# Kernel optimization log

Hardware: AMD Instinct MI355X
Metric: run time of the kernel (lower is better)

## Reference

```python
import jax, jax.numpy as jnp
import numpy as np

B, L, D, H, DH, M = 2, 2048, 512, 8, 2048, 128  # batch, seq, d_model, heads, d_hidden, max_rel_pos
HD = D // H
EPS = 1e-5


def _ln(x, w, b):
    mu = jnp.mean(x, axis=-1, keepdims=True)
    var = jnp.mean((x - mu) ** 2, axis=-1, keepdims=True)
    return (x - mu) * jax.lax.rsqrt(var + EPS) * w + b


def setup_inputs() -> dict:
    key = jax.random.key(0)
    ks = jax.random.split(key, 8)
    s = 0.02  # init std for weights
    return {
        "x": jax.random.normal(ks[0], (B, L, D), jnp.float32),
        "ln1_w": jnp.ones((D,), jnp.float32),
        "ln1_b": jnp.zeros((D,), jnp.float32),
        "qkv_w": jax.random.normal(ks[1], (D, 3 * D), jnp.float32) * s,
        "qkv_b": jnp.zeros((3 * D,), jnp.float32),
        "out_w": jax.random.normal(ks[2], (D, D), jnp.float32) * s,
        "out_b": jnp.zeros((D,), jnp.float32),
        "rel_bias": jax.random.normal(ks[3], (H, 2 * M - 1), jnp.float32) * s,
        "gamma1": 1e-4 * jnp.ones((D,), jnp.float32),
        "ln2_w": jnp.ones((D,), jnp.float32),
        "ln2_b": jnp.zeros((D,), jnp.float32),
        "ffn_in_w": jax.random.normal(ks[4], (D, 2 * DH), jnp.float32) * s,
        "ffn_in_b": jnp.zeros((2 * DH,), jnp.float32),
        "ffn_out_w": jax.random.normal(ks[5], (DH, D), jnp.float32) * s,
        "ffn_out_b": jnp.zeros((D,), jnp.float32),
        "gamma2": 1e-4 * jnp.ones((D,), jnp.float32),
    }


def _forward(x, ln1_w, ln1_b, qkv_w, qkv_b, out_w, out_b, rel_bias, gamma1,
             ln2_w, ln2_b, ffn_in_w, ffn_in_b, ffn_out_w, ffn_out_b, gamma2):
    b, l, d = x.shape
    # --- PreNorm attention with T5-style relative position bias ---
    h = _ln(x, ln1_w, ln1_b)
    qkv = h @ qkv_w + qkv_b                           # [B, L, 3D]
    q, k, v = jnp.split(qkv, 3, axis=-1)
    q = q.reshape(b, l, H, HD)
    k = k.reshape(b, l, H, HD)
    v = v.reshape(b, l, H, HD)
    scale = 1.0 / jnp.sqrt(jnp.asarray(HD, x.dtype))
    scores = jnp.einsum("bqhd,bkhd->bhqk", q, k) * scale   # [B, H, L, L]
    # relative position bias: clip(i - j) indexed into learned table
    ctx = jnp.arange(l)[:, None] - jnp.arange(l)[None, :]
    ctx = jnp.clip(ctx, -(M - 1), M - 1) + (M - 1)          # [L, L] in [0, 2M-2]
    rel = rel_bias[:, ctx]                                  # [H, L, L]
    scores = scores + rel[None]
    attn = jax.nn.softmax(scores, axis=-1)
    o = jnp.einsum("bhqk,bkhd->bqhd", attn, v).reshape(b, l, d)
    o = o @ out_w + out_b
    x = x + o * gamma1                                      # LayerScale residual
    # --- PreNorm GEGLU FFN ---
    h2 = _ln(x, ln2_w, ln2_b)
    ab = h2 @ ffn_in_w + ffn_in_b                           # [B, L, 2*DH]
    a, bgate = jnp.split(ab, 2, axis=-1)
    f = jax.nn.gelu(bgate, approximate=False) * a
    f = f @ ffn_out_w + ffn_out_b
    x = x + f * gamma2
    return x, attn


def reference(x, ln1_w, ln1_b, qkv_w, qkv_b, out_w, out_b, rel_bias, gamma1,
              ln2_w, ln2_b, ffn_in_w, ffn_in_b, ffn_out_w, ffn_out_b, gamma2):
    return _forward(x, ln1_w, ln1_b, qkv_w, qkv_b, out_w, out_b, rel_bias, gamma1,
                    ln2_w, ln2_b, ffn_in_w, ffn_in_b, ffn_out_w, ffn_out_b, gamma2)
```

## Files before the change

### kernel.cpp

```cpp
#include <hip/hip_runtime.h>
#include <math.h>

typedef __attribute__((ext_vector_type(4))) float f32x4;
typedef __attribute__((ext_vector_type(8))) short bf16x8;
typedef __attribute__((ext_vector_type(4))) short s16x4;

__device__ __forceinline__ unsigned short f2bf(float f) {
  union { float f; unsigned u; } v; v.f = f;
  return (unsigned short)((v.u + 0x7fffu + ((v.u >> 16) & 1u)) >> 16);
}

__global__ void ln_kernel(const float* __restrict__ in, const float* __restrict__ w,
                          const float* __restrict__ b, float* __restrict__ out) {
  __shared__ float sh[4];
  const int t = threadIdx.x;
  const float* p = in + (size_t)blockIdx.x * 512;
  float a0 = p[t], a1 = p[t + 256];
  float s = a0 + a1;
#pragma unroll
  for (int o = 32; o; o >>= 1) s += __shfl_down(s, o);
  if ((t & 63) == 0) sh[t >> 6] = s;
  __syncthreads();
  s = sh[0] + sh[1] + sh[2] + sh[3];
  float mu = s * (1.0f / 512.0f);
  float d0 = a0 - mu, d1 = a1 - mu;
  float q = d0 * d0 + d1 * d1;
  __syncthreads();
#pragma unroll
  for (int o = 32; o; o >>= 1) q += __shfl_down(q, o);
  if ((t & 63) == 0) sh[t >> 6] = q;
  __syncthreads();
  q = sh[0] + sh[1] + sh[2] + sh[3];
  float rstd = rsqrtf(q * (1.0f / 512.0f) + 1e-5f);
  float* po = out + (size_t)blockIdx.x * 512;
  po[t]       = d0 * rstd * w[t] + b[t];
  po[t + 256] = d1 * rstd * w[t + 256] + b[t + 256];
}

__global__ void transpose_w(const float* __restrict__ in, unsigned short* __restrict__ out,
                            int ldi, int ldo, long ibs, long obs) {
  __shared__ float tile[32][33];
  const float* ip = in + (long)blockIdx.z * ibs;
  unsigned short* op = out + (long)blockIdx.z * obs;
  const int tx = threadIdx.x & 31;
  const int ty = threadIdx.x >> 5;
  const int n0 = blockIdx.x * 32, k0 = blockIdx.y * 32;
#pragma unroll
  for (int i = 0; i < 4; ++i)
    tile[ty + i * 8][tx] = ip[(size_t)(k0 + ty + i * 8) * ldi + n0 + tx];
  __syncthreads();
#pragma unroll
  for (int i = 0; i < 4; ++i)
    op[(size_t)(n0 + ty + i * 8) * ldo + k0 + tx] = f2bf(tile[tx][ty + i * 8]);
}

template <int WM, int WN, int TM, int TN, int EPI>
__global__ __launch_bounds__(256) void gemm_kernel(
    const float* __restrict__ A, const unsigned short* __restrict__ Bt,
    float* __restrict__ C, unsigned short* __restrict__ Cbf,
    int K, int lda, int ldb, int ldc,
    const float* __restrict__ bias, const float* __restrict__ resid,
    const float* __restrict__ gamma) {
  constexpr int BM = WM * TM * 16;
  constexpr int BN = WN * TN * 16;
  __shared__ short As[BM * 32];
  __shared__ short Bs[BN * 32];

  const int tid = threadIdx.x;
  const int m0 = blockIdx.y * BM, n0 = blockIdx.x * BN;
  const int w = tid >> 6, lane = tid & 63;
  const int wm = w / WN, wn = w % WN;
  const int lrow = lane & 15, lq = lane >> 4;

  f32x4 acc[TM][TN];
#pragma unroll
  for (int i = 0; i < TM; ++i)
#pragma unroll
    for (int j = 0; j < TN; ++j) acc[i][j] = (f32x4){0.f, 0.f, 0.f, 0.f};

  for (int k0 = 0; k0 < K; k0 += 32) {
    __syncthreads();
#pragma unroll
    for (int it = 0; it < (BM * 8) / 256; ++it) {
      int c = it * 256 + tid;
      int row = c >> 3, col = (c & 7) << 2;
      float4 v = *(const float4*)(A + (size_t)(m0 + row) * lda + k0 + col);
      s16x4 r = {(short)f2bf(v.x), (short)f2bf(v.y), (short)f2bf(v.z), (short)f2bf(v.w)};
      *(s16x4*)(As + row * 32 + col) = r;
    }
#pragma unroll
    for (int it = 0; it < (BN * 4) / 256; ++it) {
      int c = it * 256 + tid;
      int row = c >> 2, col = (c & 3) << 3;
      *(bf16x8*)(Bs + row * 32 + col) =
          *(const bf16x8*)(Bt + (size_t)(n0 + row) * ldb + k0 + col);
    }
    __syncthreads();

    bf16x8 af[TM], bf[TN];
#pragma unroll
    for (int mi = 0; mi < TM; ++mi)
      af[mi] = *(const bf16x8*)(As + (wm * TM * 16 + mi * 16 + lrow) * 32 + lq * 8);
#pragma unroll
    for (int nj = 0; nj < TN; ++nj)
      bf[nj] = *(const bf16x8*)(Bs + (wn * TN * 16 + nj * 16 + lrow) * 32 + lq * 8);
#pragma unroll
    for (int mi = 0; mi < TM; ++mi)
#pragma unroll
      for (int nj = 0; nj < TN; ++nj)
        acc[mi][nj] = __builtin_amdgcn_mfma_f32_16x16x32_bf16(af[mi], bf[nj], acc[mi][nj], 0, 0, 0);
  }

#pragma unroll
  for (int mi = 0; mi < TM; ++mi) {
#pragma unroll
    for (int nj = 0; nj < TN; ++nj) {
      int gm0 = m0 + wm * TM * 16 + mi * 16 + lq * 4;
      int gn = n0 + wn * TN * 16 + nj * 16 + lrow;
#pragma unroll
      for (int r = 0; r < 4; ++r) {
        int gm = gm0 + r;
        size_t idx = (size_t)gm * ldc + gn;
        float v = acc[mi][nj][r];
        if constexpr (EPI == 0) {
          C[idx] = v + bias[gn];
        } else if constexpr (EPI == 4) {
          float u = v + bias[gn];
          C[idx] = u;
          Cbf[idx] = f2bf(u);
        } else {
          C[idx] = resid[idx] + (v + bias[gn]) * gamma[gn];
        }
      }
    }
  }
}

__global__ __launch_bounds__(256) void ffn1_gate_kernel(
    const float* __restrict__ A, const unsigned short* __restrict__ Bt,
    float* __restrict__ F, const float* __restrict__ bias) {
  __shared__ short As[128 * 32];
  __shared__ short Bs[64 * 32];
  __shared__ short Bs2[64 * 32];

  const int tid = threadIdx.x;
  const int n0 = blockIdx.x * 64, m0 = blockIdx.y * 128;
  const int w = tid >> 6, lane = tid & 63;
  const int wm = w >> 1, wn = w & 1;
  const int lrow = lane & 15, lq = lane >> 4;

  f32x4 acca[4][2], accb[4][2];
#pragma unroll
  for (int i = 0; i < 4; ++i)
#pragma unroll
    for (int j = 0; j < 2; ++j) {
      acca[i][j] = (f32x4){0.f, 0.f, 0.f, 0.f};
      accb[i][j] = (f32x4){0.f, 0.f, 0.f, 0.f};
    }

  for (int k0 = 0; k0 < 512; k0 += 32) {
    __syncthreads();
#pragma unroll
    for (int it = 0; it < 4; ++it) {
      int c = it * 256 + tid;
      int row = c >> 3, col = (c & 7) << 2;
      float4 v = *(const float4*)(A + (size_t)(m0 + row) * 512 + k0 + col);
      s16x4 r = {(short)f2bf(v.x), (short)f2bf(v.y), (short)f2bf(v.z), (short)f2bf(v.w)};
      *(s16x4*)(As + row * 32 + col) = r;
    }
    {
      int row = tid >> 2, col = (tid & 3) << 3;
      *(bf16x8*)(Bs + row * 32 + col) =
          *(const bf16x8*)(Bt + (size_t)(n0 + row) * 512 + k0 + col);
      *(bf16x8*)(Bs2 + row * 32 + col) =
          *(const bf16x8*)(Bt + (size_t)(2048 + n0 + row) * 512 + k0 + col);
    }
    __syncthreads();

    bf16x8 af[4], ba[2], bb[2];
#pragma unroll
    for (int mi = 0; mi < 4; ++mi)
      af[mi] = *(const bf16x8*)(As + (wm * 64 + mi * 16 + lrow) * 32 + lq * 8);
#pragma unroll
    for (int nj = 0; nj < 2; ++nj) {
      ba[nj] = *(const bf16x8*)(Bs + (wn * 32 + nj * 16 + lrow) * 32 + lq * 8);
      bb[nj] = *(const bf16x8*)(Bs2 + (wn * 32 + nj * 16 + lrow) * 32 + lq * 8);
    }
#pragma unroll
    for (int mi = 0; mi < 4; ++mi)
#pragma unroll
      for (int nj = 0; nj < 2; ++nj) {
        acca[mi][nj] = __builtin_amdgcn_mfma_f32_16x16x32_bf16(af[mi], ba[nj], acca[mi][nj], 0, 0, 0);
        accb[mi][nj] = __builtin_amdgcn_mfma_f32_16x16x32_bf16(af[mi], bb[nj], accb[mi][nj], 0, 0, 0);
      }
  }

#pragma unroll
  for (int mi = 0; mi < 4; ++mi)
#pragma unroll
    for (int nj = 0; nj < 2; ++nj) {
      int gm0 = m0 + wm * 64 + mi * 16 + lq * 4;
      int gn = n0 + wn * 32 + nj * 16 + lrow;
#pragma unroll
      for (int r = 0; r < 4; ++r) {
        float a = acca[mi][nj][r] + bias[gn];
        float bg = accb[mi][nj][r] + bias[2048 + gn];
        float g = 0.5f * bg * (1.0f + erff(bg * 0.70710678118654752f));
        F[(size_t)(gm0 + r) * 2048 + gn] = g * a;
      }
    }
}

__global__ __launch_bounds__(256, 4) void attn_fused(
    const unsigned short* __restrict__ qkvbf, const unsigned short* __restrict__ vt,
    const float* __restrict__ rel, float* __restrict__ attn, float* __restrict__ o) {
  __shared__ __align__(16) short p_lds[4 * 16 * 64];
  __shared__ float erel[256];
  __shared__ float rsum[32];
  __shared__ float rinv[32];

  const int tid = threadIdx.x;
  const int flat = blockIdx.y * 64 + blockIdx.x;
  const int swz = (flat & 7) * 128 + (flat >> 3);
  const int bh = swz >> 6;
  const int m0 = (swz & 63) * 32;
  const int b = bh >> 3, h = bh & 7;

  const int w = tid >> 6, lane = tid & 63;
  const int wm = w >> 1, wn = w & 1;
  const int lrow = lane & 15, lq = lane >> 4;

  const unsigned short* qb = qkvbf + (size_t)(b * 2048) * 1536 + h * 64;
  const unsigned short* kb = qb + 512;
  const unsigned short* vb = vt + (size_t)bh * 64 * 2048;
  float* ab = attn + (size_t)bh * 2048 * 2048;
  const float* relh = rel + h * 255;

  if (tid < 32) rsum[tid] = 0.f;
  if (tid < 255) erel[tid] = __expf(relh[tid]);

  bf16x8 qf[2];
#pragma unroll
  for (int c = 0; c < 2; ++c)
    qf[c] = *(const bf16x8*)(qb + (size_t)(m0 + wm * 16 + lrow) * 1536 + c * 32 + lq * 8);

  const unsigned short* krow = kb + (size_t)(wn * 64 + lrow) * 1536 + lq * 8;
  const unsigned short* vrow = vb + (size_t)lrow * 2048 + wn * 64 + lq * 8;

  const float C = 0.125f * 1.44269504088896f;

  __syncthreads();

  float psum[4] = {0.f, 0.f, 0.f, 0.f};
  const int dbase = (m0 + wm * 16 + lq * 4) - (wn * 64 + lrow);
  for (int t = 0; t < 16; ++t) {
    const int kt0 = t * 128;
    f32x4 acc[4];
#pragma unroll
    for (int nj = 0; nj < 4; ++nj) acc[nj] = (f32x4){0.f, 0.f, 0.f, 0.f};
#pragma unroll
    for (int c = 0; c < 2; ++c) {
      bf16x8 kf[4];
#pragma unroll
      for (int nj = 0; nj < 4; ++nj)
        kf[nj] = *(const bf16x8*)(krow + (size_t)(kt0 + nj * 16) * 1536 + c * 32);
#pragma unroll
      for (int nj = 0; nj < 4; ++nj)
        acc[nj] = __builtin_amdgcn_mfma_f32_16x16x32_bf16(qf[c], kf[nj], acc[nj], 0, 0, 0);
    }
    const int Dt = m0 - kt0;
    if (Dt >= 256 || Dt <= -160) {
      float ec = erel[Dt >= 256 ? 254 : 0];
#pragma unroll
      for (int r = 0; r < 4; ++r) {
        float s = 0.f;
#pragma unroll
        for (int nj = 0; nj < 4; ++nj) s += exp2f(acc[nj][r] * C);
        psum[r] += ec * s;
      }
    } else {
#pragma unroll
      for (int nj = 0; nj < 4; ++nj) {
        int d0 = dbase - kt0 - nj * 16;
#pragma unroll
        for (int r = 0; r < 4; ++r) {
          int d = d0 + r;
          d = d < -127 ? -127 : (d > 127 ? 127 : d);
          psum[r] += exp2f(acc[nj][r] * C) * erel[d + 127];
        }
      }
    }
  }
#pragma unroll
  for (int off = 1; off < 16; off <<= 1)
#pragma unroll
    for (int r = 0; r < 4; ++r) psum[r] += __shfl_xor(psum[r], off);
  if (lrow == 0) {
#pragma unroll
    for (int r = 0; r < 4; ++r) atomicAdd(&rsum[wm * 16 + lq * 4 + r], psum[r]);
  }
  __syncthreads();
  if (tid < 32) rinv[tid] = 1.0f / rsum[tid];
  __syncthreads();
  float rv[4];
#pragma unroll
  for (int r = 0; r < 4; ++r) rv[r] = rinv[wm * 16 + lq * 4 + r];

  f32x4 oacc[4];
#pragma unroll
  for (int nj = 0; nj < 4; ++nj) oacc[nj] = (f32x4){0.f, 0.f, 0.f, 0.f};
  short* pw = p_lds + w * (16 * 64);

  for (int t = 0; t < 16; ++t) {
    const int kt0 = t * 128;
    f32x4 acc[4];
#pragma unroll
    for (int nj = 0; nj < 4; ++nj) acc[nj] = (f32x4){0.f, 0.f, 0.f, 0.f};
#pragma unroll
    for (int c = 0; c < 2; ++c) {
      bf16x8 kf[4];
#pragma unroll
      for (int nj = 0; nj < 4; ++nj)
        kf[nj] = *(const bf16x8*)(krow + (size_t)(kt0 + nj * 16) * 1536 + c * 32);
#pragma unroll
      for (int nj = 0; nj < 4; ++nj)
        acc[nj] = __builtin_amdgcn_mfma_f32_16x16x32_bf16(qf[c], kf[nj], acc[nj], 0, 0, 0);
    }

    const int Dt = m0 - kt0;
    if (Dt >= 256 || Dt <= -160) {
      float ec = erel[Dt >= 256 ? 254 : 0];
#pragma unroll
      for (int r = 0; r < 4; ++r) {
        float fr = ec * rv[r];
        int prow = lq * 4 + r;
        size_t arow = (size_t)(m0 + wm * 16 + prow) * 2048 + kt0 + wn * 64 + lrow;
#pragma unroll
        for (int nj = 0; nj < 4; ++nj) {
          float e = exp2f(acc[nj][r] * C) * fr;
          __builtin_nontemporal_store(e, ab + arow + nj * 16);
          int byte = prow * 128 + ((((nj * 16 + lrow) << 1)) ^ ((prow & 7) << 4));
          *(short*)((char*)pw + byte) = (short)f2bf(e);
        }
      }
    } else {
#pragma unroll
      for (int r = 0; r < 4; ++r) {
        int prow = lq * 4 + r;
        size_t arow = (size_t)(m0 + wm * 16 + prow) * 2048 + kt0 + wn * 64 + lrow;
        int d0 = dbase - kt0 + r;
#pragma unroll
        for (int nj = 0; nj < 4; ++nj) {
          int d = d0 - nj * 16;
          d = d < -127 ? -127 : (d > 127 ? 127 : d);
          float e = exp2f(acc[nj][r] * C) * erel[d + 127] * rv[r];
          __builtin_nontemporal_store(e, ab + arow + nj * 16);
          int byte = prow * 128 + ((((nj * 16 + lrow) << 1)) ^ ((prow & 7) << 4));
          *(short*)((char*)pw + byte) = (short)f2bf(e);
        }
      }
    }

#pragma unroll
    for (int c2 = 0; c2 < 2; ++c2) {
      bf16x8 ap;
      {
        int byte = lrow * 128 + ((c2 * 64 + lq * 16) ^ ((lrow & 7) << 4));
        ap = *(const bf16x8*)((char*)pw + byte);
      }
      bf16x8 bv[4];
#pragma unroll
      for (int nj = 0; nj < 4; ++nj)
        bv[nj] = *(const bf16x8*)(vrow + (size_t)(nj * 16) * 2048 + kt0 + c2 * 32);
#pragma unroll
      for (int nj = 0; nj < 4; ++nj)
        oacc[nj] = __builtin_amdgcn_mfma_f32_16x16x32_bf16(ap, bv[nj], oacc[nj], 0, 0, 0);
    }
  }

  __syncthreads();
  float* osc = (float*)p_lds;
  if (wn == 0) {
#pragma unroll
    for (int nj = 0; nj < 4; ++nj)
#pragma unroll
      for (int r = 0; r < 4; ++r)
        osc[(wm * 16 + lq * 4 + r) * 64 + nj * 16 + lrow] = oacc[nj][r];
  }
  __syncthreads();
  if (wn == 1) {
#pragma unroll
    for (int nj = 0; nj < 4; ++nj)
#pragma unroll
      for (int r = 0; r < 4; ++r) {
        int rr = m0 + wm * 16 + lq * 4 + r;
        float v = oacc[nj][r] + osc[(wm * 16 + lq * 4 + r) * 64 + nj * 16 + lrow];
        o[(size_t)(b * 2048 + rr) * 512 + h * 64 + nj * 16 + lrow] = v;
      }
  }
}

extern "C" void kernel_launch(void* const* d_in, const int* in_sizes, int n_in,
                              void* d_out, int out_size, void* d_ws, size_t ws_size,
                              hipStream_t stream) {
  (void)in_sizes; (void)n_in; (void)out_size; (void)ws_size;
  const float* x        = (const float*)d_in[0];
  const float* ln1_w    = (const float*)d_in[1];
  const float* ln1_b    = (const float*)d_in[2];
  const float* qkv_w    = (const float*)d_in[3];
  const float* qkv_b    = (const float*)d_in[4];
  const float* out_w    = (const float*)d_in[5];
  const float* out_b    = (const float*)d_in[6];
  const float* rel_bias = (const float*)d_in[7];
  const float* gamma1   = (const float*)d_in[8];
  const float* ln2_w    = (const float*)d_in[9];
  const float* ln2_b    = (const float*)d_in[10];
  const float* ffn_in_w = (const float*)d_in[11];
  const float* ffn_in_b = (const float*)d_in[12];
  const float* ffn_out_w  = (const float*)d_in[13];
  const float* ffn_out_b  = (const float*)d_in[14];
  const float* gamma2   = (const float*)d_in[15];

  float* x_out = (float*)d_out;
  float* attn  = x_out + (size_t)2 * 2048 * 512;

  float* ws  = (float*)d_ws;
  float* h   = ws;
  float* qkv = h + 2097152;
  float* o   = qkv + 6291456;
  float* x1  = o + 2097152;
  float* f   = x1 + 2097152;
  unsigned short* bt_qkv  = (unsigned short*)(f + 8388608);
  unsigned short* bt_out  = bt_qkv + 786432;
  unsigned short* bt_ffn1 = bt_out + 262144;
  unsigned short* bt_ffn2 = bt_ffn1 + 2097152;
  unsigned short* vt      = bt_ffn2 + 1048576;
  unsigned short* qkvbf   = (unsigned short*)f;

  transpose_w<<<dim3(48, 16, 1), 256, 0, stream>>>(qkv_w,     bt_qkv,  1536, 512,  0, 0);
  transpose_w<<<dim3(16, 16, 1), 256, 0, stream>>>(out_w,     bt_out,  512,  512,  0, 0);
  transpose_w<<<dim3(128, 16, 1), 256, 0, stream>>>(ffn_in_w, bt_ffn1, 4096, 512,  0, 0);
  transpose_w<<<dim3(16, 64, 1), 256, 0, stream>>>(ffn_out_w, bt_ffn2, 512,  2048, 0, 0);

  ln_kernel<<<4096, 256, 0, stream>>>(x, ln1_w, ln1_b, h);

  gemm_kernel<2, 2, 2, 4, 4><<<dim3(12, 64, 1), 256, 0, stream>>>(
      h, bt_qkv, qkv, qkvbf, 512, 512, 512, 1536, qkv_b, nullptr, nullptr);

  transpose_w<<<dim3(2, 64, 8), 256, 0, stream>>>(
      qkv + 1024, vt, 1536, 2048, 64, (long)64 * 2048);
  transpose_w<<<dim3(2, 64, 8), 256, 0, stream>>>(
      qkv + (size_t)2048 * 1536 + 1024, vt + (size_t)8 * 64 * 2048, 1536, 2048, 64,
      (long)64 * 2048);

  attn_fused<<<dim3(64, 16, 1), 256, 0, stream>>>(qkvbf, vt, rel_bias, attn, o);

  gemm_kernel<2, 2, 2, 4, 3><<<dim3(4, 64, 1), 256, 0, stream>>>(
      o, bt_out, x1, nullptr, 512, 512, 512, 512, out_b, x, gamma1);

  ln_kernel<<<4096, 256, 0, stream>>>(x1, ln2_w, ln2_b, h);

  ffn1_gate_kernel<<<dim3(32, 32, 1), 256, 0, stream>>>(h, bt_ffn1, f, ffn_in_b);

  gemm_kernel<2, 2, 2, 4, 3><<<dim3(4, 64, 1), 256, 0, stream>>>(
      f, bt_ffn2, x_out, nullptr, 2048, 2048, 2048, 512, ffn_out_b, x1, gamma2);
}
```

Before: 601.2 us.

## Stage attention probs in fp32 LDS for vectorized stores; prescale Q into exp2 domain

The QKV epilogue now folds the softmax scale times log2(e) into the bf16 copy of Q and skips writing the unused V part of the bf16 buffer. The attention kernel then uses a raw exp2 builtin without a per-element multiply. Probabilities are staged in fp32 LDS with an XOR swizzle, so the large attn matrix can be written as 16-byte nontemporal vector stores instead of scalar ones. The bf16 conversion moves to the point where P is read back for the PV MFMA. In exchange LDS use per block doubles, which may reduce occupancy, and the extra LDS round-trip adds traffic.

```diff
diff --git a/kernel.cpp b/kernel.cpp
--- a/kernel.cpp
+++ b/kernel.cpp
@@ -4,6 +4,12 @@
 typedef __attribute__((ext_vector_type(4))) float f32x4;
 typedef __attribute__((ext_vector_type(8))) short bf16x8;
 typedef __attribute__((ext_vector_type(4))) short s16x4;
+
+#if __has_builtin(__builtin_amdgcn_exp2f)
+#define EXP2(x) __builtin_amdgcn_exp2f(x)
+#else
+#define EXP2(x) exp2f(x)
+#endif
 
 __device__ __forceinline__ unsigned short f2bf(float f) {
   union { float f; unsigned u; } v; v.f = f;
@@ -127,7 +133,8 @@
         } else if constexpr (EPI == 4) {
           float u = v + bias[gn];
           C[idx] = u;
-          Cbf[idx] = f2bf(u);
+          if (gn < 1024)
+            Cbf[idx] = f2bf(gn < 512 ? u * 0.18033688011112042f : u);
         } else {
           C[idx] = resid[idx] + (v + bias[gn]) * gamma[gn];
         }
@@ -214,7 +221,7 @@
 __global__ __launch_bounds__(256, 4) void attn_fused(
     const unsigned short* __restrict__ qkvbf, const unsigned short* __restrict__ vt,
     const float* __restrict__ rel, float* __restrict__ attn, float* __restrict__ o) {
-  __shared__ __align__(16) short p_lds[4 * 16 * 64];
+  __shared__ __align__(16) float p_f32[4 * 16 * 64];
   __shared__ float erel[256];
   __shared__ float rsum[32];
   __shared__ float rinv[32];
@@ -247,8 +254,6 @@
   const unsigned short* krow = kb + (size_t)(wn * 64 + lrow) * 1536 + lq * 8;
   const unsigned short* vrow = vb + (size_t)lrow * 2048 + wn * 64 + lq * 8;
 
-  const float C = 0.125f * 1.44269504088896f;
-
   __syncthreads();
 
   float psum[4] = {0.f, 0.f, 0.f, 0.f};
@@ -275,7 +280,7 @@
       for (int r = 0; r < 4; ++r) {
         float s = 0.f;
 #pragma unroll
-        for (int nj = 0; nj < 4; ++nj) s += exp2f(acc[nj][r] * C);
+        for (int nj = 0; nj < 4; ++nj) s += EXP2(acc[nj][r]);
         psum[r] += ec * s;
       }
     } else {
@@ -286,7 +291,7 @@
         for (int r = 0; r < 4; ++r) {
           int d = d0 + r;
           d = d < -127 ? -127 : (d > 127 ? 127 : d);
-          psum[r] += exp2f(acc[nj][r] * C) * erel[d + 127];
+          psum[r] += EXP2(acc[nj][r]) * erel[d + 127];
         }
       }
     }
@@ -309,7 +314,10 @@
   f32x4 oacc[4];
 #pragma unroll
   for (int nj = 0; nj < 4; ++nj) oacc[nj] = (f32x4){0.f, 0.f, 0.f, 0.f};
-  short* pw = p_lds + w * (16 * 64);
+  float* pw = p_f32 + w * (16 * 64);
+
+  const int wsw = lq << 4;
+  const int rsw = ((lrow >> 2) & 3) << 4;
 
   for (int t = 0; t < 16; ++t) {
     const int kt0 = t * 128;
@@ -334,40 +342,42 @@
       for (int r = 0; r < 4; ++r) {
         float fr = ec * rv[r];
         int prow = lq * 4 + r;
-        size_t arow = (size_t)(m0 + wm * 16 + prow) * 2048 + kt0 + wn * 64 + lrow;
 #pragma unroll
         for (int nj = 0; nj < 4; ++nj) {
-          float e = exp2f(acc[nj][r] * C) * fr;
-          __builtin_nontemporal_store(e, ab + arow + nj * 16);
-          int byte = prow * 128 + ((((nj * 16 + lrow) << 1)) ^ ((prow & 7) << 4));
-          *(short*)((char*)pw + byte) = (short)f2bf(e);
+          float e = EXP2(acc[nj][r]) * fr;
+          pw[prow * 64 + ((nj * 16 + lrow) ^ wsw)] = e;
         }
       }
     } else {
 #pragma unroll
       for (int r = 0; r < 4; ++r) {
         int prow = lq * 4 + r;
-        size_t arow = (size_t)(m0 + wm * 16 + prow) * 2048 + kt0 + wn * 64 + lrow;
         int d0 = dbase - kt0 + r;
 #pragma unroll
         for (int nj = 0; nj < 4; ++nj) {
           int d = d0 - nj * 16;
           d = d < -127 ? -127 : (d > 127 ? 127 : d);
-          float e = exp2f(acc[nj][r] * C) * erel[d + 127] * rv[r];
-          __builtin_nontemporal_store(e, ab + arow + nj * 16);
-          int byte = prow * 128 + ((((nj * 16 + lrow) << 1)) ^ ((prow & 7) << 4));
-          *(short*)((char*)pw + byte) = (short)f2bf(e);
+          float e = EXP2(acc[nj][r]) * (erel[d + 127] * rv[r]);
+          pw[prow * 64 + ((nj * 16 + lrow) ^ wsw)] = e;
         }
       }
     }
 
 #pragma unroll
+    for (int it = 0; it < 4; ++it) {
+      int rr = lq * 4 + it;
+      f32x4 vv = *(const f32x4*)(pw + rr * 64 + ((lrow * 4) ^ wsw));
+      __builtin_nontemporal_store(
+          vv, (f32x4*)(ab + (size_t)(m0 + wm * 16 + rr) * 2048 + kt0 + wn * 64 + lrow * 4));
+    }
+
+#pragma unroll
     for (int c2 = 0; c2 < 2; ++c2) {
-      bf16x8 ap;
-      {
-        int byte = lrow * 128 + ((c2 * 64 + lq * 16) ^ ((lrow & 7) << 4));
-        ap = *(const bf16x8*)((char*)pw + byte);
-      }
+      const float* pp = pw + lrow * 64 + ((c2 * 32 + lq * 8) ^ rsw);
+      f32x4 pa = *(const f32x4*)pp;
+      f32x4 pb = *(const f32x4*)(pp + 4);
+      bf16x8 ap = {(short)f2bf(pa[0]), (short)f2bf(pa[1]), (short)f2bf(pa[2]), (short)f2bf(pa[3]),
+                   (short)f2bf(pb[0]), (short)f2bf(pb[1]), (short)f2bf(pb[2]), (short)f2bf(pb[3])};
       bf16x8 bv[4];
 #pragma unroll
       for (int nj = 0; nj < 4; ++nj)
@@ -379,7 +389,7 @@
   }
 
   __syncthreads();
-  float* osc = (float*)p_lds;
+  float* osc = p_f32;
   if (wn == 0) {
 #pragma unroll
     for (int nj = 0; nj < 4; ++nj)
```

New measurement: 602.1 us. About the same (+0.2%).
